# Performance work log

Hardware: AMD Instinct MI355X
Metric: run time of the kernel (lower is better)

The kernel has to match this reference:

```python
import jax, jax.numpy as jnp
import numpy as np
import math

D = 512      # input_size == hidden_size
TAU = 4      # length of att/spatial lists
N = 16384    # tokens (batch*H*W)

def setup_inputs() -> dict:
    key = jax.random.key(0)
    ks = jax.random.split(key, 16)
    s = 1.0 / math.sqrt(D)
    return {
        "T_t": jax.random.normal(ks[0], (N, D), jnp.float32),
        "S_t": jax.random.normal(ks[1], (N, D), jnp.float32),
        "t_att": jax.random.normal(ks[2], (TAU, N, D), jnp.float32),
        "s_att": jax.random.normal(ks[3], (TAU, N, D), jnp.float32),
        "t_spatial": jax.random.normal(ks[4], (TAU, N, D), jnp.float32),
        "s_spatial": jax.random.normal(ks[5], (TAU, N, D), jnp.float32),
        # fl_t: Linear(D, 3D); fl_t_next: Linear(D, D); same for s
        "W_t": jax.random.uniform(ks[6], (3 * D, D), jnp.float32, -s, s),
        "b_t": jax.random.uniform(ks[7], (3 * D,), jnp.float32, -s, s),
        "W_tn": jax.random.uniform(ks[8], (D, D), jnp.float32, -s, s),
        "b_tn": jax.random.uniform(ks[9], (D,), jnp.float32, -s, s),
        "W_s": jax.random.uniform(ks[10], (3 * D, D), jnp.float32, -s, s),
        "b_s": jax.random.uniform(ks[11], (3 * D,), jnp.float32, -s, s),
        "W_sn": jax.random.uniform(ks[12], (D, D), jnp.float32, -s, s),
        "b_sn": jax.random.uniform(ks[13], (D,), jnp.float32, -s, s),
    }

def reference(T_t, S_t, t_att, s_att, t_spatial, s_spatial,
              W_t, b_t, W_tn, b_tn, W_s, b_s, W_sn, b_sn):
    d = T_t.shape[-1]
    scale = 1.0 / jnp.sqrt(jnp.asarray(d, T_t.dtype))
    s_next = S_t @ W_sn.T + b_sn          # [N, D]
    t_next = T_t @ W_tn.T + b_tn          # [N, D]

    # trend weights: dot-product along feature dim, softmax over tau axis
    w_s = jax.nn.softmax(jnp.einsum('knd,nd->kn', s_att, s_next) * scale, axis=0)
    w_t = jax.nn.softmax(jnp.einsum('knd,nd->kn', t_spatial, t_next) * scale, axis=0)
    T_trend = jnp.einsum('knd,kn->nd', t_att, w_s)      # [N, D]
    S_trend = jnp.einsum('knd,kn->nd', s_spatial, w_t)  # [N, D]

    t_gate = jax.nn.sigmoid(t_next)
    s_gate = jax.nn.sigmoid(s_next)
    T_fusion = T_t * t_gate + (1.0 - t_gate) * T_trend
    S_fusion = S_t * s_gate + (1.0 - s_gate) * S_trend

    T_concat = T_fusion @ W_t.T + b_t     # [N, 3D]
    S_concat = S_fusion @ W_s.T + b_s
    t_g, t_t, t_s = jnp.split(T_concat, 3, axis=1)
    s_g, s_t, s_s = jnp.split(S_concat, 3, axis=1)
    T_gate = jax.nn.sigmoid(t_g)
    S_gate = jax.nn.sigmoid(s_g)
    T_new = T_gate * t_t + (1.0 - T_gate) * s_t
    S_new = S_gate * s_s + (1.0 - S_gate) * t_s
    return T_new, S_new
```

## Files before the change

### kernel.cpp

```cpp
#include <hip/hip_runtime.h>

#define NTOK 16384
#define DIM 512
#define NTAU 4

typedef __attribute__((ext_vector_type(4))) float f32x4;
typedef __attribute__((ext_vector_type(8))) short bf16x8;
typedef __attribute__((ext_vector_type(4))) unsigned short u16x4;
typedef __attribute__((ext_vector_type(8))) unsigned short u16x8;

__device__ inline unsigned short f2bf(float f) {
    union { float f; unsigned int u; } v; v.f = f;
    unsigned int u = v.u + 0x7FFFu + ((v.u >> 16) & 1u);
    return (unsigned short)(u >> 16);
}

__device__ inline void bf8_to_f32(u16x8 h, f32x4& a, f32x4& b) {
    union { unsigned int u; float f; } t;
#pragma unroll
    for (int e = 0; e < 4; e++) { t.u = ((unsigned int)h[e]) << 16; a[e] = t.f; }
#pragma unroll
    for (int e = 0; e < 4; e++) { t.u = ((unsigned int)h[4 + e]) << 16; b[e] = t.f; }
}

#define NTLOAD4(p) __builtin_nontemporal_load((const f32x4*)(p))

__global__ void convert_f32_bf16(const float* __restrict__ src,
                                 unsigned short* __restrict__ dst, int n4) {
    int i = blockIdx.x * blockDim.x + threadIdx.x;
    if (i < n4) {
        f32x4 v = ((const f32x4*)src)[i];
        u16x4 o;
        o[0] = f2bf(v[0]); o[1] = f2bf(v[1]); o[2] = f2bf(v[2]); o[3] = f2bf(v[3]);
        ((u16x4*)dst)[i] = o;
    }
}

__global__ __launch_bounds__(256, 2) void gemm_next(
    const float* __restrict__ A, const unsigned short* __restrict__ W,
    const float* __restrict__ bias, unsigned short* __restrict__ out)
{
    __shared__ unsigned short lA[128][40];
    __shared__ unsigned short lB[128][40];
    const int tid = threadIdx.x;
    const int m0 = blockIdx.y * 128;
    const int n0 = blockIdx.x * 128;
    const int lane = tid & 63;
    const int w = tid >> 6;
    const int wr = w >> 1, wc = w & 1;

    f32x4 acc[4][4];
#pragma unroll
    for (int i = 0; i < 4; i++)
#pragma unroll
        for (int j = 0; j < 4; j++) acc[i][j] = (f32x4){0.f, 0.f, 0.f, 0.f};

    const int arow = tid >> 3;
    const int acol = (tid & 7) * 4;
    const int brow = tid >> 2;
    const int bcol = (tid & 3) * 8;

    for (int k0 = 0; k0 < DIM; k0 += 32) {
#pragma unroll
        for (int i = 0; i < 4; i++) {
            int r = arow + 32 * i;
            f32x4 v = *(const f32x4*)(A + (size_t)(m0 + r) * DIM + k0 + acol);
            u16x4 o;
            o[0] = f2bf(v[0]); o[1] = f2bf(v[1]); o[2] = f2bf(v[2]); o[3] = f2bf(v[3]);
            *(u16x4*)&lA[r][acol] = o;
        }
#pragma unroll
        for (int i = 0; i < 2; i++) {
            int r = brow + 64 * i;
            u16x8 v = *(const u16x8*)(W + (size_t)(n0 + r) * DIM + k0 + bcol);
            *(u16x8*)&lB[r][bcol] = v;
        }
        __syncthreads();

        bf16x8 af[4], bfr[4];
#pragma unroll
        for (int i = 0; i < 4; i++)
            af[i] = *(const bf16x8*)&lA[wr * 64 + i * 16 + (lane & 15)][(lane >> 4) * 8];
#pragma unroll
        for (int j = 0; j < 4; j++)
            bfr[j] = *(const bf16x8*)&lB[wc * 64 + j * 16 + (lane & 15)][(lane >> 4) * 8];
#pragma unroll
        for (int i = 0; i < 4; i++)
#pragma unroll
            for (int j = 0; j < 4; j++)
                acc[i][j] = __builtin_amdgcn_mfma_f32_16x16x32_bf16(af[i], bfr[j], acc[i][j], 0, 0, 0);
        __syncthreads();
    }

#pragma unroll
    for (int j = 0; j < 4; j++) {
        int n = n0 + wc * 64 + j * 16 + (lane & 15);
        float bv = bias[n];
#pragma unroll
        for (int i = 0; i < 4; i++) {
            int mbase = m0 + wr * 64 + i * 16 + (lane >> 4) * 4;
#pragma unroll
            for (int r = 0; r < 4; r++)
                out[(size_t)(mbase + r) * DIM + n] = f2bf(acc[i][j][r] + bv);
        }
    }
}

__global__ __launch_bounds__(256) void fuse_stream(
    const float* __restrict__ T_t, const float* __restrict__ S_t,
    const float* __restrict__ t_att, const float* __restrict__ s_att,
    const float* __restrict__ t_spatial, const float* __restrict__ s_spatial,
    const unsigned short* __restrict__ t_next, const unsigned short* __restrict__ s_next,
    unsigned short* __restrict__ Tf, unsigned short* __restrict__ Sf)
{
    const int lane = threadIdx.x & 63;
    const int w = blockIdx.x * 4 + (threadIdx.x >> 6);
    const float scale = 0.04419417382415922f;
    const int c = lane * 8;

    const int n[2] = { 2 * w, 2 * w + 1 };
    f32x4 tn_a[2], tn_b[2], sn_a[2], sn_b[2];
#pragma unroll
    for (int t = 0; t < 2; t++) {
        const size_t rb = (size_t)n[t] * DIM + c;
        bf8_to_f32(*(const u16x8*)(t_next + rb), tn_a[t], tn_b[t]);
        bf8_to_f32(*(const u16x8*)(s_next + rb), sn_a[t], sn_b[t]);
    }

    float dws[2][NTAU], dwt[2][NTAU];
#pragma unroll
    for (int t = 0; t < 2; t++) {
#pragma unroll
        for (int k = 0; k < NTAU; k++) {
            const size_t kb = ((size_t)k * NTOK + n[t]) * DIM + c;
            f32x4 sa = NTLOAD4(s_att + kb);
            f32x4 sb = NTLOAD4(s_att + kb + 4);
            f32x4 ta = NTLOAD4(t_spatial + kb);
            f32x4 tb = NTLOAD4(t_spatial + kb + 4);
            dws[t][k] = sa[0]*sn_a[t][0]+sa[1]*sn_a[t][1]+sa[2]*sn_a[t][2]+sa[3]*sn_a[t][3]
                      + sb[0]*sn_b[t][0]+sb[1]*sn_b[t][1]+sb[2]*sn_b[t][2]+sb[3]*sn_b[t][3];
            dwt[t][k] = ta[0]*tn_a[t][0]+ta[1]*tn_a[t][1]+ta[2]*tn_a[t][2]+ta[3]*tn_a[t][3]
                      + tb[0]*tn_b[t][0]+tb[1]*tn_b[t][1]+tb[2]*tn_b[t][2]+tb[3]*tn_b[t][3];
        }
    }
#pragma unroll
    for (int t = 0; t < 2; t++)
#pragma unroll
        for (int k = 0; k < NTAU; k++) {
            float v = dws[t][k];
#pragma unroll
            for (int off = 32; off; off >>= 1) v += __shfl_xor(v, off);
            dws[t][k] = v * scale;
            float u = dwt[t][k];
#pragma unroll
            for (int off = 32; off; off >>= 1) u += __shfl_xor(u, off);
            dwt[t][k] = u * scale;
        }

    float ws_[2][NTAU], wt_[2][NTAU];
#pragma unroll
    for (int t = 0; t < 2; t++) {
        float ms = fmaxf(fmaxf(dws[t][0], dws[t][1]), fmaxf(dws[t][2], dws[t][3]));
        float mt = fmaxf(fmaxf(dwt[t][0], dwt[t][1]), fmaxf(dwt[t][2], dwt[t][3]));
        float ssum = 0.f, tsum = 0.f;
#pragma unroll
        for (int k = 0; k < NTAU; k++) {
            ws_[t][k] = __expf(dws[t][k] - ms); ssum += ws_[t][k];
            wt_[t][k] = __expf(dwt[t][k] - mt); tsum += wt_[t][k];
        }
        float rs = 1.f / ssum, rt = 1.f / tsum;
#pragma unroll
        for (int k = 0; k < NTAU; k++) { ws_[t][k] *= rs; wt_[t][k] *= rt; }
    }

#pragma unroll
    for (int t = 0; t < 2; t++) {
        const size_t rb = (size_t)n[t] * DIM + c;
        f32x4 Tta = {0,0,0,0}, Ttb = {0,0,0,0}, Sta = {0,0,0,0}, Stb = {0,0,0,0};
#pragma unroll
        for (int k = 0; k < NTAU; k++) {
            const size_t kb = ((size_t)k * NTOK + n[t]) * DIM + c;
            f32x4 ta = NTLOAD4(t_att + kb);
            f32x4 tb = NTLOAD4(t_att + kb + 4);
            f32x4 sa = NTLOAD4(s_spatial + kb);
            f32x4 sb = NTLOAD4(s_spatial + kb + 4);
            float wk = ws_[t][k], vk = wt_[t][k];
#pragma unroll
            for (int e = 0; e < 4; e++) {
                Tta[e] += wk * ta[e]; Ttb[e] += wk * tb[e];
                Sta[e] += vk * sa[e]; Stb[e] += vk * sb[e];
            }
        }
        f32x4 Ta = *(const f32x4*)(T_t + rb);
        f32x4 Tb = *(const f32x4*)(T_t + rb + 4);
        f32x4 Sa = *(const f32x4*)(S_t + rb);
        f32x4 Sb = *(const f32x4*)(S_t + rb + 4);

        u16x8 oT, oS;
#pragma unroll
        for (int e = 0; e < 4; e++) {
            float gt_a = 1.f / (1.f + __expf(-tn_a[t][e]));
            float gt_b = 1.f / (1.f + __expf(-tn_b[t][e]));
            float gs_a = 1.f / (1.f + __expf(-sn_a[t][e]));
            float gs_b = 1.f / (1.f + __expf(-sn_b[t][e]));
            oT[e]     = f2bf(Ta[e] * gt_a + (1.f - gt_a) * Tta[e]);
            oT[4 + e] = f2bf(Tb[e] * gt_b + (1.f - gt_b) * Ttb[e]);
            oS[e]     = f2bf(Sa[e] * gs_a + (1.f - gs_a) * Sta[e]);
            oS[4 + e] = f2bf(Sb[e] * gs_b + (1.f - gs_b) * Stb[e]);
        }
        *(u16x8*)(Tf + rb) = oT;
        *(u16x8*)(Sf + rb) = oS;
    }
}

__global__ __launch_bounds__(256, 2) void gemm_final(
    const unsigned short* __restrict__ Tf, const unsigned short* __restrict__ Sf,
    const unsigned short* __restrict__ Wt, const unsigned short* __restrict__ Ws,
    const float* __restrict__ bt, const float* __restrict__ bs,
    float* __restrict__ out)
{
    __shared__ unsigned short lT[128][40];
    __shared__ unsigned short lS[128][40];
    __shared__ unsigned short lW[6][32][40];
    const int tid = threadIdx.x;
    const int m0 = blockIdx.y * 128;
    const int j0 = blockIdx.x * 32;
    const int lane = tid & 63;
    const int w = tid >> 6, wr = w >> 1, wc = w & 1;

    f32x4 acc[6][4];
#pragma unroll
    for (int g = 0; g < 6; g++)
#pragma unroll
        for (int i = 0; i < 4; i++) acc[g][i] = (f32x4){0.f, 0.f, 0.f, 0.f};

    const int arow = tid >> 2;
    const int acol = (tid & 3) * 8;

    for (int k0 = 0; k0 < DIM; k0 += 32) {
#pragma unroll
        for (int i = 0; i < 2; i++) {
            int r = arow + 64 * i;
            *(u16x8*)&lT[r][acol] = *(const u16x8*)(Tf + (size_t)(m0 + r) * DIM + k0 + acol);
            *(u16x8*)&lS[r][acol] = *(const u16x8*)(Sf + (size_t)(m0 + r) * DIM + k0 + acol);
        }
#pragma unroll
        for (int i = 0; i < 3; i++) {
            int cidx = tid + 256 * i;
            int g = cidx >> 7;
            int rr = (cidx >> 2) & 31;
            int ch = (cidx & 3) * 8;
            const unsigned short* src = (g < 3) ? Wt : Ws;
            int row = (g % 3) * DIM + j0 + rr;
            *(u16x8*)&lW[g][rr][ch] = *(const u16x8*)(src + (size_t)row * DIM + k0 + ch);
        }
        __syncthreads();

        bf16x8 aT[4], aS[4];
#pragma unroll
        for (int i = 0; i < 4; i++) {
            aT[i] = *(const bf16x8*)&lT[wr * 64 + i * 16 + (lane & 15)][(lane >> 4) * 8];
            aS[i] = *(const bf16x8*)&lS[wr * 64 + i * 16 + (lane & 15)][(lane >> 4) * 8];
        }
#pragma unroll
        for (int g = 0; g < 6; g++) {
            bf16x8 bw = *(const bf16x8*)&lW[g][wc * 16 + (lane & 15)][(lane >> 4) * 8];
#pragma unroll
            for (int i = 0; i < 4; i++)
                acc[g][i] = __builtin_amdgcn_mfma_f32_16x16x32_bf16(
                    (g < 3) ? aT[i] : aS[i], bw, acc[g][i], 0, 0, 0);
        }
        __syncthreads();
    }

    const int j = j0 + wc * 16 + (lane & 15);
    const float btg = bt[j], btt = bt[512 + j], bts = bt[1024 + j];
    const float bsg = bs[j], bst = bs[512 + j], bss = bs[1024 + j];
#pragma unroll
    for (int i = 0; i < 4; i++) {
        int mbase = m0 + wr * 64 + i * 16 + (lane >> 4) * 4;
#pragma unroll
        for (int r = 0; r < 4; r++) {
            float TG = acc[0][i][r] + btg;
            float TT = acc[1][i][r] + btt;
            float TS = acc[2][i][r] + bts;
            float SG = acc[3][i][r] + bsg;
            float ST = acc[4][i][r] + bst;
            float SS = acc[5][i][r] + bss;
            float gT = 1.f / (1.f + __expf(-TG));
            float gS = 1.f / (1.f + __expf(-SG));
            size_t m = (size_t)(mbase + r);
            out[m * DIM + j] = gT * TT + (1.f - gT) * ST;
            out[(size_t)NTOK * DIM + m * DIM + j] = gS * SS + (1.f - gS) * TS;
        }
    }
}

extern "C" void kernel_launch(void* const* d_in, const int* in_sizes, int n_in,
                              void* d_out, int out_size, void* d_ws, size_t ws_size,
                              hipStream_t stream) {
    const float* T_t       = (const float*)d_in[0];
    const float* S_t       = (const float*)d_in[1];
    const float* t_att     = (const float*)d_in[2];
    const float* s_att     = (const float*)d_in[3];
    const float* t_spatial = (const float*)d_in[4];
    const float* s_spatial = (const float*)d_in[5];
    const float* W_t  = (const float*)d_in[6];
    const float* b_t  = (const float*)d_in[7];
    const float* W_tn = (const float*)d_in[8];
    const float* b_tn = (const float*)d_in[9];
    const float* W_s  = (const float*)d_in[10];
    const float* b_s  = (const float*)d_in[11];
    const float* W_sn = (const float*)d_in[12];
    const float* b_sn = (const float*)d_in[13];
    float* out = (float*)d_out;

    char* ws = (char*)d_ws;
    unsigned short* t_next = (unsigned short*)(ws + 0);
    unsigned short* s_next = (unsigned short*)(ws + 16777216);
    unsigned short* Tf     = (unsigned short*)(ws + 33554432);
    unsigned short* Sf     = (unsigned short*)(ws + 50331648);
    unsigned short* Wtn_b  = (unsigned short*)(ws + 67108864);
    unsigned short* Wsn_b  = (unsigned short*)(ws + 67633152);
    unsigned short* Wt_b   = (unsigned short*)(ws + 68157440);
    unsigned short* Ws_b   = (unsigned short*)(ws + 69730304);

    const int n_sq = 512 * 512 / 4, n_big = 1536 * 512 / 4;
    convert_f32_bf16<<<(n_sq + 255) / 256, 256, 0, stream>>>(W_tn, Wtn_b, n_sq);
    convert_f32_bf16<<<(n_sq + 255) / 256, 256, 0, stream>>>(W_sn, Wsn_b, n_sq);
    convert_f32_bf16<<<(n_big + 255) / 256, 256, 0, stream>>>(W_t, Wt_b, n_big);
    convert_f32_bf16<<<(n_big + 255) / 256, 256, 0, stream>>>(W_s, Ws_b, n_big);

    dim3 g1(DIM / 128, NTOK / 128);
    gemm_next<<<g1, 256, 0, stream>>>(T_t, Wtn_b, b_tn, t_next);
    gemm_next<<<g1, 256, 0, stream>>>(S_t, Wsn_b, b_sn, s_next);

    fuse_stream<<<2048, 256, 0, stream>>>(T_t, S_t, t_att, s_att, t_spatial, s_spatial,
                                          t_next, s_next, Tf, Sf);

    dim3 g3(DIM / 32, NTOK / 128);
    gemm_final<<<g3, 256, 0, stream>>>(Tf, Sf, Wt_b, Ws_b, b_t, b_s, out);
}
```

Measured before the change: 305.8 us.

## Remap GEMM tiles per XCD and restructure fuse_stream to issue all loads early

```diff
diff --git a/kernel.cpp b/kernel.cpp
--- a/kernel.cpp
+++ b/kernel.cpp
@@ -43,8 +43,11 @@
     __shared__ unsigned short lA[128][40];
     __shared__ unsigned short lB[128][40];
     const int tid = threadIdx.x;
-    const int m0 = blockIdx.y * 128;
-    const int n0 = blockIdx.x * 128;
+    const int id = blockIdx.x + 4 * blockIdx.y;
+    const int xcd = id & 7;
+    const int idx = id >> 3;
+    const int m0 = (xcd * 16 + (idx >> 2)) * 128;
+    const int n0 = (idx & 3) * 128;
     const int lane = tid & 63;
     const int w = tid >> 6;
     const int wr = w >> 1, wc = w & 1;
@@ -114,103 +117,102 @@
     unsigned short* __restrict__ Tf, unsigned short* __restrict__ Sf)
 {
     const int lane = threadIdx.x & 63;
-    const int w = blockIdx.x * 4 + (threadIdx.x >> 6);
+    const int n = (blockIdx.x << 2) + (threadIdx.x >> 6);
+    const int c = lane * 8;
+    const size_t rb = (size_t)n * DIM + c;
     const float scale = 0.04419417382415922f;
-    const int c = lane * 8;
-
-    const int n[2] = { 2 * w, 2 * w + 1 };
-    f32x4 tn_a[2], tn_b[2], sn_a[2], sn_b[2];
-#pragma unroll
-    for (int t = 0; t < 2; t++) {
-        const size_t rb = (size_t)n[t] * DIM + c;
-        bf8_to_f32(*(const u16x8*)(t_next + rb), tn_a[t], tn_b[t]);
-        bf8_to_f32(*(const u16x8*)(s_next + rb), sn_a[t], sn_b[t]);
-    }
-
-    float dws[2][NTAU], dwt[2][NTAU];
-#pragma unroll
-    for (int t = 0; t < 2; t++) {
+
+    f32x4 tn_a, tn_b, sn_a, sn_b;
+    bf8_to_f32(*(const u16x8*)(t_next + rb), tn_a, tn_b);
+    bf8_to_f32(*(const u16x8*)(s_next + rb), sn_a, sn_b);
+
+    f32x4 p1s[NTAU][2], p1t[NTAU][2];
+#pragma unroll
+    for (int k = 0; k < NTAU; k++) {
+        const size_t kb = ((size_t)k * NTOK + n) * DIM + c;
+        p1s[k][0] = NTLOAD4(s_att + kb);
+        p1s[k][1] = NTLOAD4(s_att + kb + 4);
+        p1t[k][0] = NTLOAD4(t_spatial + kb);
+        p1t[k][1] = NTLOAD4(t_spatial + kb + 4);
+    }
+
+    float dws[NTAU], dwt[NTAU];
+#pragma unroll
+    for (int k = 0; k < NTAU; k++) {
+        f32x4 a0 = p1s[k][0], a1 = p1s[k][1];
+        f32x4 b0 = p1t[k][0], b1 = p1t[k][1];
+        dws[k] = a0[0]*sn_a[0]+a0[1]*sn_a[1]+a0[2]*sn_a[2]+a0[3]*sn_a[3]
+               + a1[0]*sn_b[0]+a1[1]*sn_b[1]+a1[2]*sn_b[2]+a1[3]*sn_b[3];
+        dwt[k] = b0[0]*tn_a[0]+b0[1]*tn_a[1]+b0[2]*tn_a[2]+b0[3]*tn_a[3]
+               + b1[0]*tn_b[0]+b1[1]*tn_b[1]+b1[2]*tn_b[2]+b1[3]*tn_b[3];
+    }
+
+    f32x4 p2t[NTAU][2], p2s[NTAU][2];
+#pragma unroll
+    for (int k = 0; k < NTAU; k++) {
+        const size_t kb = ((size_t)k * NTOK + n) * DIM + c;
+        p2t[k][0] = NTLOAD4(t_att + kb);
+        p2t[k][1] = NTLOAD4(t_att + kb + 4);
+        p2s[k][0] = NTLOAD4(s_spatial + kb);
+        p2s[k][1] = NTLOAD4(s_spatial + kb + 4);
+    }
+    f32x4 Ta = *(const f32x4*)(T_t + rb);
+    f32x4 Tb = *(const f32x4*)(T_t + rb + 4);
+    f32x4 Sa = *(const f32x4*)(S_t + rb);
+    f32x4 Sb = *(const f32x4*)(S_t + rb + 4);
+
+#pragma unroll
+    for (int k = 0; k < NTAU; k++) {
+        float v = dws[k];
+#pragma unroll
+        for (int off = 32; off; off >>= 1) v += __shfl_xor(v, off);
+        dws[k] = v * scale;
+        float u = dwt[k];
+#pragma unroll
+        for (int off = 32; off; off >>= 1) u += __shfl_xor(u, off);
+        dwt[k] = u * scale;
+    }
+
+    float ws_[NTAU], wt_[NTAU];
+    {
+        float ms = fmaxf(fmaxf(dws[0], dws[1]), fmaxf(dws[2], dws[3]));
+        float mt = fmaxf(fmaxf(dwt[0], dwt[1]), fmaxf(dwt[2], dwt[3]));
+        float ssum = 0.f, tsum = 0.f;
 #pragma unroll
         for (int k = 0; k < NTAU; k++) {
-            const size_t kb = ((size_t)k * NTOK + n[t]) * DIM + c;
-            f32x4 sa = NTLOAD4(s_att + kb);
-            f32x4 sb = NTLOAD4(s_att + kb + 4);
-            f32x4 ta = NTLOAD4(t_spatial + kb);
-            f32x4 tb = NTLOAD4(t_spatial + kb + 4);
-            dws[t][k] = sa[0]*sn_a[t][0]+sa[1]*sn_a[t][1]+sa[2]*sn_a[t][2]+sa[3]*sn_a[t][3]
-                      + sb[0]*sn_b[t][0]+sb[1]*sn_b[t][1]+sb[2]*sn_b[t][2]+sb[3]*sn_b[t][3];
-            dwt[t][k] = ta[0]*tn_a[t][0]+ta[1]*tn_a[t][1]+ta[2]*tn_a[t][2]+ta[3]*tn_a[t][3]
-                      + tb[0]*tn_b[t][0]+tb[1]*tn_b[t][1]+tb[2]*tn_b[t][2]+tb[3]*tn_b[t][3];
-        }
-    }
-#pragma unroll
-    for (int t = 0; t < 2; t++)
-#pragma unroll
-        for (int k = 0; k < NTAU; k++) {
-            float v = dws[t][k];
-#pragma unroll
-            for (int off = 32; off; off >>= 1) v += __shfl_xor(v, off);
-            dws[t][k] = v * scale;
-            float u = dwt[t][k];
-#pragma unroll
-            for (int off = 32; off; off >>= 1) u += __shfl_xor(u, off);
-            dwt[t][k] = u * scale;
-        }
-
-    float ws_[2][NTAU], wt_[2][NTAU];
-#pragma unroll
-    for (int t = 0; t < 2; t++) {
-        float ms = fmaxf(fmaxf(dws[t][0], dws[t][1]), fmaxf(dws[t][2], dws[t][3]));
-        float mt = fmaxf(fmaxf(dwt[t][0], dwt[t][1]), fmaxf(dwt[t][2], dwt[t][3]));
-        float ssum = 0.f, tsum = 0.f;
-#pragma unroll
-        for (int k = 0; k < NTAU; k++) {
-            ws_[t][k] = __expf(dws[t][k] - ms); ssum += ws_[t][k];
-            wt_[t][k] = __expf(dwt[t][k] - mt); tsum += wt_[t][k];
+            ws_[k] = __expf(dws[k] - ms); ssum += ws_[k];
+            wt_[k] = __expf(dwt[k] - mt); tsum += wt_[k];
         }
         float rs = 1.f / ssum, rt = 1.f / tsum;
 #pragma unroll
-        for (int k = 0; k < NTAU; k++) { ws_[t][k] *= rs; wt_[t][k] *= rt; }
-    }
-
-#pragma unroll
-    for (int t = 0; t < 2; t++) {
-        const size_t rb = (size_t)n[t] * DIM + c;
-        f32x4 Tta = {0,0,0,0}, Ttb = {0,0,0,0}, Sta = {0,0,0,0}, Stb = {0,0,0,0};
-#pragma unroll
-        for (int k = 0; k < NTAU; k++) {
-            const size_t kb = ((size_t)k * NTOK + n[t]) * DIM + c;
-            f32x4 ta = NTLOAD4(t_att + kb);
-            f32x4 tb = NTLOAD4(t_att + kb + 4);
-            f32x4 sa = NTLOAD4(s_spatial + kb);
-            f32x4 sb = NTLOAD4(s_spatial + kb + 4);
-            float wk = ws_[t][k], vk = wt_[t][k];
-#pragma unroll
-            for (int e = 0; e < 4; e++) {
-                Tta[e] += wk * ta[e]; Ttb[e] += wk * tb[e];
-                Sta[e] += vk * sa[e]; Stb[e] += vk * sb[e];
-            }
-        }
-        f32x4 Ta = *(const f32x4*)(T_t + rb);
-        f32x4 Tb = *(const f32x4*)(T_t + rb + 4);
-        f32x4 Sa = *(const f32x4*)(S_t + rb);
-        f32x4 Sb = *(const f32x4*)(S_t + rb + 4);
-
-        u16x8 oT, oS;
+        for (int k = 0; k < NTAU; k++) { ws_[k] *= rs; wt_[k] *= rt; }
+    }
+
+    f32x4 Tta = {0,0,0,0}, Ttb = {0,0,0,0}, Sta = {0,0,0,0}, Stb = {0,0,0,0};
+#pragma unroll
+    for (int k = 0; k < NTAU; k++) {
+        float wk = ws_[k], vk = wt_[k];
 #pragma unroll
         for (int e = 0; e < 4; e++) {
-            float gt_a = 1.f / (1.f + __expf(-tn_a[t][e]));
-            float gt_b = 1.f / (1.f + __expf(-tn_b[t][e]));
-            float gs_a = 1.f / (1.f + __expf(-sn_a[t][e]));
-            float gs_b = 1.f / (1.f + __expf(-sn_b[t][e]));
-            oT[e]     = f2bf(Ta[e] * gt_a + (1.f - gt_a) * Tta[e]);
-            oT[4 + e] = f2bf(Tb[e] * gt_b + (1.f - gt_b) * Ttb[e]);
-            oS[e]     = f2bf(Sa[e] * gs_a + (1.f - gs_a) * Sta[e]);
-            oS[4 + e] = f2bf(Sb[e] * gs_b + (1.f - gs_b) * Stb[e]);
-        }
-        *(u16x8*)(Tf + rb) = oT;
-        *(u16x8*)(Sf + rb) = oS;
-    }
+            Tta[e] += wk * p2t[k][0][e]; Ttb[e] += wk * p2t[k][1][e];
+            Sta[e] += vk * p2s[k][0][e]; Stb[e] += vk * p2s[k][1][e];
+        }
+    }
+
+    u16x8 oT, oS;
+#pragma unroll
+    for (int e = 0; e < 4; e++) {
+        float gt_a = 1.f / (1.f + __expf(-tn_a[e]));
+        float gt_b = 1.f / (1.f + __expf(-tn_b[e]));
+        float gs_a = 1.f / (1.f + __expf(-sn_a[e]));
+        float gs_b = 1.f / (1.f + __expf(-sn_b[e]));
+        oT[e]     = f2bf(Ta[e] * gt_a + (1.f - gt_a) * Tta[e]);
+        oT[4 + e] = f2bf(Tb[e] * gt_b + (1.f - gt_b) * Ttb[e]);
+        oS[e]     = f2bf(Sa[e] * gs_a + (1.f - gs_a) * Sta[e]);
+        oS[4 + e] = f2bf(Sb[e] * gs_b + (1.f - gs_b) * Stb[e]);
+    }
+    *(u16x8*)(Tf + rb) = oT;
+    *(u16x8*)(Sf + rb) = oS;
 }
 
 __global__ __launch_bounds__(256, 2) void gemm_final(
@@ -223,8 +225,11 @@
     __shared__ unsigned short lS[128][40];
     __shared__ unsigned short lW[6][32][40];
     const int tid = threadIdx.x;
-    const int m0 = blockIdx.y * 128;
-    const int j0 = blockIdx.x * 32;
+    const int id = blockIdx.x + 16 * blockIdx.y;
+    const int xcd = id & 7;
+    const int idx = id >> 3;
+    const int m0 = (xcd * 16 + (idx >> 4)) * 128;
+    const int j0 = (idx & 15) * 32;
     const int lane = tid & 63;
     const int w = tid >> 6, wr = w >> 1, wc = w & 1;
 
@@ -335,7 +340,7 @@
     gemm_next<<<g1, 256, 0, stream>>>(T_t, Wtn_b, b_tn, t_next);
     gemm_next<<<g1, 256, 0, stream>>>(S_t, Wsn_b, b_sn, s_next);
 
-    fuse_stream<<<2048, 256, 0, stream>>>(T_t, S_t, t_att, s_att, t_spatial, s_spatial,
+    fuse_stream<<<4096, 256, 0, stream>>>(T_t, S_t, t_att, s_att, t_spatial, s_spatial,
                                           t_next, s_next, Tf, Sf);
 
     dim3 g3(DIM / 32, NTOK / 128);
```

Result: faster. 292.5 us (-4.4%).
